# Performance work log

Measured on AMD Instinct MI355X. Metric: run time of the kernel, lower is better.

The kernel has to match this reference:

```python
import jax, jax.numpy as jnp
import numpy as np

N_NODES = 50000
N_EDGES = 800000
FEAT_DIM = 1024
EMBED_DIM = 128


def setup_inputs() -> dict:
    key = jax.random.key(0)
    k_x, k_w, k_r, k_c, k_v = jax.random.split(key, 5)
    x = jax.random.normal(k_x, (N_NODES, FEAT_DIM), dtype=jnp.float32)
    # xavier-uniform equivalent for weight [embed_dim, feat_dim]
    limit = float(np.sqrt(6.0 / (EMBED_DIM + FEAT_DIM)))
    weight = jax.random.uniform(k_w, (EMBED_DIM, FEAT_DIM), dtype=jnp.float32,
                                minval=-limit, maxval=limit)
    # sparse adjacency in COO form (row = destination, col = source)
    adj_row = jax.random.randint(k_r, (N_EDGES,), 0, N_NODES, dtype=jnp.int32)
    adj_col = jax.random.randint(k_c, (N_EDGES,), 0, N_NODES, dtype=jnp.int32)
    adj_vals = jax.random.uniform(k_v, (N_EDGES,), dtype=jnp.float32)
    return {"x": x, "weight": weight, "adj_row": adj_row,
            "adj_col": adj_col, "adj_vals": adj_vals}


def reference(x, weight, adj_row, adj_col, adj_vals):
    # Fused GeMM-SpMM: out = A @ (x @ W^T)
    h = jnp.einsum('nf,ef->ne', x, weight)          # [N, embed_dim] dense GEMM
    msgs = adj_vals[:, None] * h[adj_col]           # gather source rows, scale by edge weight
    out = jax.ops.segment_sum(msgs, adj_row, num_segments=N_NODES)  # scatter-add to dest rows
    return out
```

## Files before the change

kernel.cpp:

```cpp
#include <hip/hip_runtime.h>
#include <hip/hip_bf16.h>

#define FEAT 1024
#define EMBED 128
#define CAP 64
#define OVF_CAP 4096

#define NCHUNK 16
#define B_CHUNK 16384

typedef __attribute__((ext_vector_type(8))) short short8;
typedef __attribute__((ext_vector_type(4))) float floatx4;

__device__ inline ushort f2bf(float f) {
    __hip_bfloat16 h = __float2bfloat16(f);
    return *reinterpret_cast<ushort*>(&h);
}
__device__ inline float bfbits_lo(uint u) {
    uint v = u << 16; return *reinterpret_cast<float*>(&v);
}
__device__ inline float bfbits_hi(uint u) {
    uint v = u & 0xffff0000u; return *reinterpret_cast<float*>(&v);
}

__device__ inline void async_copy16(const void* g, void* l) {
    __builtin_amdgcn_global_load_lds(
        (const __attribute__((address_space(1))) void*)g,
        (__attribute__((address_space(3))) void*)l, 16, 0, 0);
}

__global__ void swizzle_weight_kernel(const float* __restrict__ w,
                                      ushort* __restrict__ wbs) {
    int gid = blockIdx.x * blockDim.x + threadIdx.x;
    int l = gid & 63;
    int t = (gid >> 6) & 7;
    int s = gid >> 9;
    int row = t * 16 + (l & 15);
    int col = s * 32 + (l >> 4) * 8;
    const float* src = w + (size_t)row * FEAT + col;
    float4 v0 = *(const float4*)(src);
    float4 v1 = *(const float4*)(src + 4);
    short8 o;
    o[0] = f2bf(v0.x); o[1] = f2bf(v0.y); o[2] = f2bf(v0.z); o[3] = f2bf(v0.w);
    o[4] = f2bf(v1.x); o[5] = f2bf(v1.y); o[6] = f2bf(v1.z); o[7] = f2bf(v1.w);
    *(short8*)(wbs + (size_t)gid * 8) = o;
}

__launch_bounds__(256, 3)
__global__ void gemm_bucket_kernel(const float* __restrict__ x,
                                   const ushort* __restrict__ wbs,
                                   ushort* __restrict__ hb, int n_nodes,
                                   const int* __restrict__ adj_row,
                                   const int* __restrict__ adj_col,
                                   const float* __restrict__ adj_vals,
                                   int* __restrict__ cnt,
                                   int2* __restrict__ bucket,
                                   int* __restrict__ ovf_cnt,
                                   int* __restrict__ ovf_list,
                                   int n_edges, int gemm_blocks, int bucket_blocks) {
    __shared__ __align__(16) char lds[2][B_CHUNK];

    if (blockIdx.x >= gemm_blocks) {
        int stride = bucket_blocks * 256;
        for (int e = (blockIdx.x - gemm_blocks) * 256 + threadIdx.x;
             e < n_edges; e += stride) {
            int r = adj_row[e];
            int slot = atomicAdd(&cnt[r], 1);
            if (slot < CAP) {
                bucket[(size_t)r * CAP + slot] =
                    make_int2(adj_col[e], __float_as_int(adj_vals[e]));
            } else {
                int oi = atomicAdd(ovf_cnt, 1);
                if (oi < OVF_CAP) ovf_list[oi] = e;
            }
        }
        return;
    }

    const int lane = threadIdx.x & 63;
    const int wave = threadIdx.x >> 6;
    const int q    = lane >> 4;
    const int m    = lane & 15;
    const int base = blockIdx.x * 64 + wave * 16;

    int row = base + m;
    if (row >= n_nodes) row = n_nodes - 1;
    const float* xp = x + (size_t)row * FEAT + q * 8;
    const char* wbb = (const char*)wbs;

    {
        const char* bs = wbb + wave * 4096 + lane * 16;
        char* bd = lds[0] + wave * 4096;
#pragma unroll
        for (int k = 0; k < 4; ++k)
            async_copy16(bs + k * 1024, bd + k * 1024);
    }

    float4 A0 = *(const float4*)(xp);
    float4 A1 = *(const float4*)(xp + 4);
    float4 A2 = *(const float4*)(xp + 32);
    float4 A3 = *(const float4*)(xp + 36);

    floatx4 acc[8];
#pragma unroll
    for (int t = 0; t < 8; ++t) acc[t] = (floatx4)(0.0f);

    __syncthreads();

    for (int c = 0; c < NCHUNK; ++c) {
        const char* buf = lds[c & 1];
        float4 N0, N1, N2, N3;
        if (c + 1 < NCHUNK) {
            const char* bs = wbb + (size_t)(c + 1) * B_CHUNK + wave * 4096 + lane * 16;
            char* bd = lds[(c + 1) & 1] + wave * 4096;
#pragma unroll
            for (int k = 0; k < 4; ++k)
                async_copy16(bs + k * 1024, bd + k * 1024);
            const float* np = xp + (c + 1) * 64;
            N0 = *(const float4*)(np);
            N1 = *(const float4*)(np + 4);
            N2 = *(const float4*)(np + 32);
            N3 = *(const float4*)(np + 36);
        }
#pragma unroll
        for (int sl = 0; sl < 2; ++sl) {
            const char* bsrc = buf + sl * 8192 + lane * 16;
            short8 bf[8];
#pragma unroll
            for (int t = 0; t < 8; ++t) bf[t] = *(const short8*)(bsrc + t * 1024);

            float4 al = sl ? A2 : A0;
            float4 ah = sl ? A3 : A1;
            short8 af;
            af[0] = f2bf(al.x); af[1] = f2bf(al.y);
            af[2] = f2bf(al.z); af[3] = f2bf(al.w);
            af[4] = f2bf(ah.x); af[5] = f2bf(ah.y);
            af[6] = f2bf(ah.z); af[7] = f2bf(ah.w);

#pragma unroll
            for (int t = 0; t < 8; ++t)
                acc[t] = __builtin_amdgcn_mfma_f32_16x16x32_bf16(af, bf[t], acc[t], 0, 0, 0);
        }
        __syncthreads();
        A0 = N0; A1 = N1; A2 = N2; A3 = N3;
    }

#pragma unroll
    for (int t = 0; t < 8; ++t) {
#pragma unroll
        for (int r = 0; r < 4; ++r) {
            int rr = base + q * 4 + r;
            if (rr < n_nodes)
                hb[(size_t)rr * EMBED + t * 16 + m] = f2bf(acc[t][r]);
        }
    }
}

__launch_bounds__(256)
__global__ void gather_kernel(const int* __restrict__ cnt,
                              const int2* __restrict__ bucket,
                              const ushort* __restrict__ hb,
                              const int* __restrict__ ovf_cnt,
                              const int* __restrict__ ovf_list,
                              const int* __restrict__ adj_row,
                              const int* __restrict__ adj_col,
                              const float* __restrict__ adj_vals,
                              float* __restrict__ out, int n_nodes) {
    int node = __builtin_amdgcn_readfirstlane(blockIdx.x * 4 + (threadIdx.x >> 6));
    if (node >= n_nodes) return;
    int lane = threadIdx.x & 63;
    int c_raw = cnt[node];
    int c = c_raw > CAP ? CAP : c_raw;
    const int2* bp = bucket + (size_t)node * CAP;
    const ushort* hl = hb + lane * 2;

    float accx = 0.0f, accy = 0.0f;
    int nb = c >> 4;
    if (nb > 0) {
        int4 eb[8];
#pragma unroll
        for (int i = 0; i < 8; ++i) eb[i] = *(const int4*)(bp + i * 2);
        for (int b = 0; b < nb; ++b) {
            uint u[16]; float wv[16];
#pragma unroll
            for (int i = 0; i < 8; ++i) {
                u[2*i]   = *(const uint*)(hl + (size_t)eb[i].x * EMBED);
                u[2*i+1] = *(const uint*)(hl + (size_t)eb[i].z * EMBED);
                wv[2*i]   = __int_as_float(eb[i].y);
                wv[2*i+1] = __int_as_float(eb[i].w);
            }
            if (b + 1 < nb) {
#pragma unroll
                for (int i = 0; i < 8; ++i)
                    eb[i] = *(const int4*)(bp + (b + 1) * 16 + i * 2);
            }
#pragma unroll
            for (int i = 0; i < 16; ++i) {
                accx = fmaf(wv[i], bfbits_lo(u[i]), accx);
                accy = fmaf(wv[i], bfbits_hi(u[i]), accy);
            }
        }
    }
    int j = nb * 16;
    if (j + 8 <= c) {
        int4 eb[4];
#pragma unroll
        for (int i = 0; i < 4; ++i) eb[i] = *(const int4*)(bp + j + i * 2);
        uint u[8]; float wv[8];
#pragma unroll
        for (int i = 0; i < 4; ++i) {
            u[2*i]   = *(const uint*)(hl + (size_t)eb[i].x * EMBED);
            u[2*i+1] = *(const uint*)(hl + (size_t)eb[i].z * EMBED);
            wv[2*i]   = __int_as_float(eb[i].y);
            wv[2*i+1] = __int_as_float(eb[i].w);
        }
#pragma unroll
        for (int i = 0; i < 8; ++i) {
            accx = fmaf(wv[i], bfbits_lo(u[i]), accx);
            accy = fmaf(wv[i], bfbits_hi(u[i]), accy);
        }
        j += 8;
    }
    for (; j + 2 <= c; j += 2) {
        int4 e01 = *(const int4*)(bp + j);
        uint u0 = *(const uint*)(hl + (size_t)e01.x * EMBED);
        uint u1 = *(const uint*)(hl + (size_t)e01.z * EMBED);
        float w0 = __int_as_float(e01.y), w1 = __int_as_float(e01.w);
        accx = fmaf(w0, bfbits_lo(u0), accx);  accy = fmaf(w0, bfbits_hi(u0), accy);
        accx = fmaf(w1, bfbits_lo(u1), accx);  accy = fmaf(w1, bfbits_hi(u1), accy);
    }
    if (j < c) {
        int2 ev = bp[j];
        uint u = *(const uint*)(hl + (size_t)ev.x * EMBED);
        float w = __int_as_float(ev.y);
        accx = fmaf(w, bfbits_lo(u), accx);
        accy = fmaf(w, bfbits_hi(u), accy);
    }
    if (c_raw > CAP) {
        int n = *ovf_cnt;
        if (n > OVF_CAP) n = OVF_CAP;
        for (int i = 0; i < n; ++i) {
            int e = ovf_list[i];
            if (adj_row[e] == node) {
                uint u = *(const uint*)(hl + (size_t)adj_col[e] * EMBED);
                float w = adj_vals[e];
                accx = fmaf(w, bfbits_lo(u), accx);
                accy = fmaf(w, bfbits_hi(u), accy);
            }
        }
    }
    *(float2*)(out + (size_t)node * EMBED + lane * 2) = make_float2(accx, accy);
}

extern "C" void kernel_launch(void* const* d_in, const int* in_sizes, int n_in,
                              void* d_out, int out_size, void* d_ws, size_t ws_size,
                              hipStream_t stream) {
    const float* x        = (const float*)d_in[0];
    const float* w        = (const float*)d_in[1];
    const int*   adj_row  = (const int*)d_in[2];
    const int*   adj_col  = (const int*)d_in[3];
    const float* adj_vals = (const float*)d_in[4];

    const int n_nodes = in_sizes[0] / FEAT;
    const int n_edges = in_sizes[2];
    float* out = (float*)d_out;

    char* ws = (char*)d_ws;
    ushort* wbs = (ushort*)ws;
    size_t off = 262144;
    ushort* hb = (ushort*)(ws + off);
    off += (size_t)n_nodes * EMBED * sizeof(ushort);
    char* meta = ws + off;
    int* cnt      = (int*)meta;
    int* ovf_cnt  = (int*)(meta + (size_t)n_nodes * 4);
    int* ovf_list = ovf_cnt + 1;
    size_t meta_bytes = ((size_t)n_nodes * 4 + 4 + OVF_CAP * 4 + 15) & ~(size_t)15;
    int2* bucket = (int2*)(meta + meta_bytes);

    hipMemsetAsync(meta, 0, meta_bytes, stream);

    swizzle_weight_kernel<<<64, 256, 0, stream>>>(w, wbs);

    const int gemm_blocks   = (n_nodes + 63) / 64;
    const int bucket_blocks = 1024;
    gemm_bucket_kernel<<<gemm_blocks + bucket_blocks, 256, 0, stream>>>(
        x, wbs, hb, n_nodes,
        adj_row, adj_col, adj_vals,
        cnt, bucket, ovf_cnt, ovf_list, n_edges, gemm_blocks, bucket_blocks);

    gather_kernel<<<(n_nodes + 3) / 4, 256, 0, stream>>>(
        cnt, bucket, hb, ovf_cnt, ovf_list, adj_row, adj_col, adj_vals,
        out, n_nodes);
}
```

Baseline: 365.1 us.

## Split bucket fill from GEMM and stage X tiles through swizzled LDS

The edge-bucketing work moves out of the fused GEMM launch into its own kernel. The GEMM kernel now loads X with coalesced row-contiguous float4 reads and writes them into an XOR-swizzled LDS tile. It also DMAs larger 32KB weight chunks per stage and pipelines with explicit vmcnt waits and barriers. The goal is to fix the strided per-lane X reads and improve memory-level parallelism. The cost is much more LDS, which limits occupancy to one block per CU, and the loss of overlap between bucketing and the GEMM.

```diff
diff --git a/kernel.cpp b/kernel.cpp
--- a/kernel.cpp
+++ b/kernel.cpp
@@ -6,9 +6,6 @@
 #define CAP 64
 #define OVF_CAP 4096
 
-#define NCHUNK 16
-#define B_CHUNK 16384
-
 typedef __attribute__((ext_vector_type(8))) short short8;
 typedef __attribute__((ext_vector_type(4))) float floatx4;
 
@@ -27,6 +24,14 @@
     __builtin_amdgcn_global_load_lds(
         (const __attribute__((address_space(1))) void*)g,
         (__attribute__((address_space(3))) void*)l, 16, 0, 0);
+}
+__device__ inline void wait_vm8() {
+    asm volatile("s_waitcnt vmcnt(8)" ::: "memory");
+    __builtin_amdgcn_sched_barrier(0);
+}
+__device__ inline void wait_vm0() {
+    asm volatile("s_waitcnt vmcnt(0)" ::: "memory");
+    __builtin_amdgcn_sched_barrier(0);
 }
 
 __global__ void swizzle_weight_kernel(const float* __restrict__ w,
@@ -46,36 +51,32 @@
     *(short8*)(wbs + (size_t)gid * 8) = o;
 }
 
-__launch_bounds__(256, 3)
-__global__ void gemm_bucket_kernel(const float* __restrict__ x,
-                                   const ushort* __restrict__ wbs,
-                                   ushort* __restrict__ hb, int n_nodes,
-                                   const int* __restrict__ adj_row,
+__global__ void bucket_fill_kernel(const int* __restrict__ adj_row,
                                    const int* __restrict__ adj_col,
                                    const float* __restrict__ adj_vals,
                                    int* __restrict__ cnt,
                                    int2* __restrict__ bucket,
                                    int* __restrict__ ovf_cnt,
                                    int* __restrict__ ovf_list,
-                                   int n_edges, int gemm_blocks, int bucket_blocks) {
-    __shared__ __align__(16) char lds[2][B_CHUNK];
-
-    if (blockIdx.x >= gemm_blocks) {
-        int stride = bucket_blocks * 256;
-        for (int e = (blockIdx.x - gemm_blocks) * 256 + threadIdx.x;
-             e < n_edges; e += stride) {
-            int r = adj_row[e];
-            int slot = atomicAdd(&cnt[r], 1);
-            if (slot < CAP) {
-                bucket[(size_t)r * CAP + slot] =
-                    make_int2(adj_col[e], __float_as_int(adj_vals[e]));
-            } else {
-                int oi = atomicAdd(ovf_cnt, 1);
-                if (oi < OVF_CAP) ovf_list[oi] = e;
-            }
-        }
-        return;
-    }
+                                   int n_edges) {
+    int e = blockIdx.x * blockDim.x + threadIdx.x;
+    if (e >= n_edges) return;
+    int r = adj_row[e];
+    int slot = atomicAdd(&cnt[r], 1);
+    if (slot < CAP) {
+        bucket[(size_t)r * CAP + slot] = make_int2(adj_col[e], __float_as_int(adj_vals[e]));
+    } else {
+        int oi = atomicAdd(ovf_cnt, 1);
+        if (oi < OVF_CAP) ovf_list[oi] = e;
+    }
+}
+
+__launch_bounds__(256, 1)
+__global__ void gemm_xwT_kernel(const float* __restrict__ x,
+                                const ushort* __restrict__ wbs,
+                                ushort* __restrict__ hb, int n_nodes) {
+    __shared__ __align__(16) char Alds[4 * 2 * 8192];
+    __shared__ __align__(16) char Blds[32768];
 
     const int lane = threadIdx.x & 63;
     const int wave = threadIdx.x >> 6;
@@ -83,67 +84,103 @@
     const int m    = lane & 15;
     const int base = blockIdx.x * 64 + wave * 16;
 
-    int row = base + m;
-    if (row >= n_nodes) row = n_nodes - 1;
-    const float* xp = x + (size_t)row * FEAT + q * 8;
+    const char* xb  = (const char*)x;
     const char* wbb = (const char*)wbs;
 
-    {
-        const char* bs = wbb + wave * 4096 + lane * 16;
-        char* bd = lds[0] + wave * 4096;
-#pragma unroll
-        for (int k = 0; k < 4; ++k)
-            async_copy16(bs + k * 1024, bd + k * 1024);
-    }
-
-    float4 A0 = *(const float4*)(xp);
-    float4 A1 = *(const float4*)(xp + 4);
-    float4 A2 = *(const float4*)(xp + 32);
-    float4 A3 = *(const float4*)(xp + 36);
+    const int rl_half = lane >> 5;
+    const int cb      = (lane & 31) * 16;
+    uint arow[8];
+#pragma unroll
+    for (int i = 0; i < 8; ++i) {
+        int rl = 2 * i + rl_half;
+        int rg = base + rl;
+        if (rg >= n_nodes) rg = n_nodes - 1;
+        arow[i] = (uint)rg * (FEAT * 4) + cb;
+    }
+
+    float4 Areg[8];
+#define A_LOAD(oct_) do {                                                     \
+        _Pragma("unroll")                                                     \
+        for (int i = 0; i < 8; ++i)                                           \
+            Areg[i] = *(const float4*)(xb + (size_t)arow[i] + (oct_) * 512);  \
+    } while (0)
+
+#define A_WRITE(oct_) do {                                                    \
+        char* Ab_ = Alds + (wave * 2 + ((oct_) & 1)) * 8192;                  \
+        _Pragma("unroll")                                                     \
+        for (int i = 0; i < 8; ++i) {                                         \
+            int rl_ = 2 * i + rl_half;                                        \
+            *(float4*)(Ab_ + rl_ * 512 + (cb ^ ((rl_ & 7) << 4))) = Areg[i];  \
+        }                                                                     \
+    } while (0)
+
+#define B_DMA(oct_) do {                                                      \
+        const char* bs_ = wbb + (size_t)(oct_) * 32768 + wave * 8192 + lane * 16; \
+        char* bd_ = Blds + wave * 8192;                                       \
+        _Pragma("unroll")                                                     \
+        for (int k = 0; k < 8; ++k)                                           \
+            async_copy16(bs_ + k * 1024, bd_ + k * 1024);                     \
+    } while (0)
 
     floatx4 acc[8];
 #pragma unroll
     for (int t = 0; t < 8; ++t) acc[t] = (floatx4)(0.0f);
 
-    __syncthreads();
-
-    for (int c = 0; c < NCHUNK; ++c) {
-        const char* buf = lds[c & 1];
-        float4 N0, N1, N2, N3;
-        if (c + 1 < NCHUNK) {
-            const char* bs = wbb + (size_t)(c + 1) * B_CHUNK + wave * 4096 + lane * 16;
-            char* bd = lds[(c + 1) & 1] + wave * 4096;
-#pragma unroll
-            for (int k = 0; k < 4; ++k)
-                async_copy16(bs + k * 1024, bd + k * 1024);
-            const float* np = xp + (c + 1) * 64;
-            N0 = *(const float4*)(np);
-            N1 = *(const float4*)(np + 4);
-            N2 = *(const float4*)(np + 32);
-            N3 = *(const float4*)(np + 36);
-        }
-#pragma unroll
-        for (int sl = 0; sl < 2; ++sl) {
-            const char* bsrc = buf + sl * 8192 + lane * 16;
+    A_LOAD(0);
+    wait_vm0();
+    A_WRITE(0);
+    B_DMA(0);
+    A_LOAD(1);
+    wait_vm8();
+    asm volatile("s_waitcnt lgkmcnt(0)" ::: "memory");
+    __builtin_amdgcn_sched_barrier(0);
+    __builtin_amdgcn_s_barrier();
+
+    const int xk = (m & 7) << 4;
+#pragma unroll
+    for (int o = 0; o < 8; ++o) {
+        const char* Ab = Alds + (wave * 2 + (o & 1)) * 8192;
+#pragma unroll
+        for (int sl = 0; sl < 4; ++sl) {
+            float4 alo = *(const float4*)(Ab + m * 512 + ((sl * 128 + q * 32)      ^ xk));
+            float4 ahi = *(const float4*)(Ab + m * 512 + ((sl * 128 + q * 32 + 16) ^ xk));
+            const char* bsrc = Blds + sl * 8192 + lane * 16;
             short8 bf[8];
 #pragma unroll
             for (int t = 0; t < 8; ++t) bf[t] = *(const short8*)(bsrc + t * 1024);
 
-            float4 al = sl ? A2 : A0;
-            float4 ah = sl ? A3 : A1;
             short8 af;
-            af[0] = f2bf(al.x); af[1] = f2bf(al.y);
-            af[2] = f2bf(al.z); af[3] = f2bf(al.w);
-            af[4] = f2bf(ah.x); af[5] = f2bf(ah.y);
-            af[6] = f2bf(ah.z); af[7] = f2bf(ah.w);
+            af[0] = f2bf(alo.x); af[1] = f2bf(alo.y);
+            af[2] = f2bf(alo.z); af[3] = f2bf(alo.w);
+            af[4] = f2bf(ahi.x); af[5] = f2bf(ahi.y);
+            af[6] = f2bf(ahi.z); af[7] = f2bf(ahi.w);
 
 #pragma unroll
             for (int t = 0; t < 8; ++t)
                 acc[t] = __builtin_amdgcn_mfma_f32_16x16x32_bf16(af, bf[t], acc[t], 0, 0, 0);
         }
-        __syncthreads();
-        A0 = N0; A1 = N1; A2 = N2; A3 = N3;
-    }
+
+        if (o < 7) {
+            asm volatile("s_waitcnt lgkmcnt(0)" ::: "memory");
+            __builtin_amdgcn_sched_barrier(0);
+            __builtin_amdgcn_s_barrier();
+            B_DMA(o + 1);
+            wait_vm8();
+            A_WRITE(o + 1);
+            if (o < 6) {
+                A_LOAD(o + 2);
+                wait_vm8();
+            } else {
+                wait_vm0();
+            }
+            asm volatile("s_waitcnt lgkmcnt(0)" ::: "memory");
+            __builtin_amdgcn_sched_barrier(0);
+            __builtin_amdgcn_s_barrier();
+        }
+    }
+#undef A_LOAD
+#undef A_WRITE
+#undef B_DMA
 
 #pragma unroll
     for (int t = 0; t < 8; ++t) {
@@ -279,14 +316,12 @@
 
     hipMemsetAsync(meta, 0, meta_bytes, stream);
 
+    bucket_fill_kernel<<<(n_edges + 255) / 256, 256, 0, stream>>>(
+        adj_row, adj_col, adj_vals, cnt, bucket, ovf_cnt, ovf_list, n_edges);
+
     swizzle_weight_kernel<<<64, 256, 0, stream>>>(w, wbs);
 
-    const int gemm_blocks   = (n_nodes + 63) / 64;
-    const int bucket_blocks = 1024;
-    gemm_bucket_kernel<<<gemm_blocks + bucket_blocks, 256, 0, stream>>>(
-        x, wbs, hb, n_nodes,
-        adj_row, adj_col, adj_vals,
-        cnt, bucket, ovf_cnt, ovf_list, n_edges, gemm_blocks, bucket_blocks);
+    gemm_xwT_kernel<<<(n_nodes + 63) / 64, 256, 0, stream>>>(x, wbs, hb, n_nodes);
 
     gather_kernel<<<(n_nodes + 3) / 4, 256, 0, stream>>>(
         cnt, bucket, hb, ovf_cnt, ovf_list, adj_row, adj_col, adj_vals,
```

Result: slower. 428.3 us (+17.3%).
